# Performance work log

Hardware: AMD Instinct MI355X
Metric: run time of the kernel (lower is better)

## Reference

```python
import jax, jax.numpy as jnp
import numpy as np

U, S, D, ORDER, R, B = 339, 5825, 128, 3, 32, 500000
N = U + S
NNZ = 200000
H = D // 2  # MLP hidden = dimension // 2 = 64
EPS = 1e-5


def _xavier(key, shape):
    lim = (6.0 / (shape[0] + shape[1])) ** 0.5
    return jax.random.uniform(key, shape, minval=-lim, maxval=lim, dtype=jnp.float32)


def setup_inputs() -> dict:
    key = jax.random.key(0)
    ks = jax.random.split(key, 16)
    # --- sparse bipartite adjacency (binary, symmetrized, sym-normalized) ---
    rng = np.random.default_rng(0)
    flat = rng.choice(U * S, size=NNZ, replace=False)
    u = (flat // S).astype(np.int64)
    s = (flat % S).astype(np.int64) + U
    rows = np.concatenate([u, s])
    cols = np.concatenate([s, u])
    deg = np.bincount(rows, minlength=N).astype(np.float32)
    dinv = np.where(deg > 0, deg ** -0.5, 0.0).astype(np.float32)
    vals = dinv[rows] * dinv[cols]
    inp = {
        'uEmbeds': _xavier(ks[0], (U, D)),
        'iEmbeds': _xavier(ks[1], (S, D)),
        'uHyper': _xavier(ks[2], (R, D)),
        'iHyper': _xavier(ks[3], (R, D)),
        'W1': _xavier(ks[4], (2 * D, H)), 'b1': jnp.zeros((H,), jnp.float32),
        'g1': jnp.ones((H,), jnp.float32), 'be1': jnp.zeros((H,), jnp.float32),
        'W2': _xavier(ks[5], (H, H)), 'b2': jnp.zeros((H,), jnp.float32),
        'g2': jnp.ones((H,), jnp.float32), 'be2': jnp.zeros((H,), jnp.float32),
        'W3': _xavier(ks[6], (H, 1)), 'b3': jnp.zeros((1,), jnp.float32),
        'adj_vals': jnp.asarray(vals),
        'adj_rows': jnp.asarray(rows, dtype=jnp.int32),
        'adj_cols': jnp.asarray(cols, dtype=jnp.int32),
        'userIdx': jax.random.randint(ks[7], (B,), 0, U, dtype=jnp.int32),
        'servIdx': jax.random.randint(ks[8], (B,), 0, S, dtype=jnp.int32),
    }
    return inp


def _layernorm(x, g, b):
    mu = jnp.mean(x, axis=-1, keepdims=True)
    var = jnp.var(x, axis=-1, keepdims=True)
    return (x - mu) * jax.lax.rsqrt(var + EPS) * g + b


def reference(uEmbeds, iEmbeds, uHyper, iHyper,
              W1, b1, g1, be1, W2, b2, g2, be2, W3, b3,
              adj_vals, adj_rows, adj_cols, userIdx, servIdx):
    # multi-order GCN propagation via sparse COO spmm
    embeds = jnp.concatenate([uEmbeds, iEmbeds], axis=0)  # [N, D]
    for _ in range(ORDER):
        embeds = jax.ops.segment_sum(adj_vals[:, None] * embeds[adj_cols],
                                     adj_rows, num_segments=N)
    # hypergraph projection (embeds are detached in the original)
    e = jax.lax.stop_gradient(embeds)
    hyperU = e[:U] @ (uHyper.T @ uHyper)   # [U, D]
    hyperI = e[U:] @ (iHyper.T @ iHyper)   # [S, D]
    x = jnp.concatenate([hyperU[userIdx], hyperI[servIdx]], axis=1)  # [B, 2D]
    h = jax.nn.relu(_layernorm(x @ W1 + b1, g1, be1))
    h = jax.nn.relu(_layernorm(h @ W2 + b2, g2, be2))
    return h @ W3 + b3  # [B, 1]
```

## Files before the change

### kernel.cpp

```cpp
#include <hip/hip_runtime.h>
#include <hip/hip_bf16.h>

#define U_CNT 339
#define S_CNT 5825
#define N_CNT 6164
#define D_DIM 128
#define R_DIM 32
#define B_CNT 500000
#define NNZ_U 200000
#define H_DIM 64
#define LN_EPS 1e-5f

#define SPAD 5856
#define UPAD 352
#define KT_S 183
#define KT_U 11
#define NT_S 365
#define NT_U 22
#define U_KCHUNK 23

#define ET_U16 (D_DIM * SPAD)
#define PKS_U16 (KT_U * NT_S * 512)
#define PKU_U16 (KT_S * NT_U * 512)
#define WT_U16  (H_DIM * UPAD)
#define GU_U16  (UPAD * UPAD)
#define V_U16   (KT_U * 8 * 512)

#define PRE_S_UNITS 183
#define PRE_U_UNITS 11
#define PRE_UT_END (PRE_S_UNITS + PRE_U_UNITS)
#define PRE_EDGE_UNITS ((NNZ_U + 255) / 256)
#define PRE_UNITS (PRE_UT_END + PRE_EDGE_UNITS)

#define HV_GU_END 484
#define HV_YT_END 660
#define HV_BLOCKS 669

#define WF_B1   4096
#define WF_G1   4160
#define WF_BE1  4224
#define WF_B2   4288
#define WF_G2   4352
#define WF_BE2  4416
#define WF_W3   4480
#define WF_B3   4544
#define WF_TOT  4545

#define MLP_BLOCKS 1024

typedef __hip_bfloat16 bf16;
typedef __attribute__((ext_vector_type(8))) short sh8;
typedef __attribute__((ext_vector_type(4))) float f4v;

__device__ __forceinline__ float b2f(bf16 x) { return __bfloat162float(x); }
__device__ __forceinline__ unsigned short f2bs(float f) {
    union { bf16 b; unsigned short s; } u;
    u.b = __float2bfloat16(f);
    return u.s;
}
__device__ __forceinline__ float bu2f(unsigned int lo16) {
    return __uint_as_float(lo16 << 16);
}
__device__ __forceinline__ float ldf(const void* p, long i, int isf32) {
    return isf32 ? ((const float*)p)[i] : b2f(((const bf16*)p)[i]);
}
__device__ __forceinline__ int detect_f32(const void* uE) {
    const unsigned short* p = (const unsigned short*)uE;
    int lane = threadIdx.x & 63;
    unsigned short v = p[2 * lane];
    int e = (v >> 7) & 0xFF;
    unsigned long long m = __ballot(e >= 127);
    return (m != 0ull) ? 1 : 0;
}

template<int CTRL>
__device__ __forceinline__ float dpp_add(float x) {
    int t = __builtin_amdgcn_update_dpp(0, __float_as_int(x), CTRL, 0xF, 0xF, false);
    return x + __int_as_float(t);
}
__device__ __forceinline__ float rowsum16(float x) {
    x = dpp_add<0xB1>(x);
    x = dpp_add<0x4E>(x);
    x = dpp_add<0x124>(x);
    x = dpp_add<0x128>(x);
    return x;
}

__global__ void __launch_bounds__(256)
k_pre(const void* __restrict__ iE,
      unsigned short* __restrict__ EtHi, unsigned short* __restrict__ EtLo,
      const int* __restrict__ rows, const int* __restrict__ cols,
      const void* __restrict__ vals,
      unsigned short* __restrict__ PkS, unsigned short* __restrict__ PkU,
      float* __restrict__ uEt,
      const void* __restrict__ uE) {
    __shared__ float ls[32 * 129];
    int tid = threadIdx.x;
    int isf32 = detect_f32(uE);
    int unit = blockIdx.x;
    if (unit < PRE_S_UNITS) {
        int sg0 = unit * 32;
        int nl = tid >> 3, dbase = (tid & 7) * 16;
        int s = sg0 + nl;
        #pragma unroll
        for (int i = 0; i < 16; ++i) {
            int d = dbase + i;
            float v = (s < S_CNT) ? ldf(iE, (long)s * D_DIM + d, isf32) : 0.f;
            ls[nl * 129 + d] = v;
        }
        __syncthreads();
        int nl2 = tid & 31;
        int s2 = sg0 + nl2;
        #pragma unroll
        for (int i = 0; i < 16; ++i) {
            int d = (tid >> 5) * 16 + i;
            float v = ls[nl2 * 129 + d];
            unsigned short hi = f2bs(v);
            unsigned short lo = f2bs(v - bu2f(hi));
            EtHi[(size_t)d * SPAD + s2] = hi;
            EtLo[(size_t)d * SPAD + s2] = lo;
        }
    } else if (unit < PRE_UT_END) {
        int ug0 = (unit - PRE_S_UNITS) * 32;
        int nl = tid >> 3, dbase = (tid & 7) * 16;
        int u = ug0 + nl;
        #pragma unroll
        for (int i = 0; i < 16; ++i) {
            int d = dbase + i;
            float v = (u < U_CNT) ? ldf(uE, (long)u * D_DIM + d, isf32) : 0.f;
            ls[nl * 129 + d] = v;
        }
        __syncthreads();
        int nl2 = tid & 31;
        int u2 = ug0 + nl2;
        #pragma unroll
        for (int i = 0; i < 16; ++i) {
            int d = (tid >> 5) * 16 + i;
            uEt[(size_t)d * UPAD + u2] = (u2 < UPAD) ? ls[nl2 * 129 + d] : 0.f;
        }
    } else {
        int e = (unit - PRE_UT_END) * 256 + tid;
        if (e < NNZ_U) {
            int r = rows[e];
            if (r < U_CNT) {
                int u = r, s = cols[e] - U_CNT;
                unsigned short w = f2bs(ldf(vals, e, isf32));
                int kt = u >> 5, kq = (u >> 3) & 3, j = u & 7;
                int nt = s >> 4, nn = s & 15;
                PkS[((kt * NT_S + nt) * 64 + kq * 16 + nn) * 8 + j] = w;
                int kt2 = s >> 5, kq2 = (s >> 3) & 3, j2 = s & 7;
                int nt2 = u >> 4, nn2 = u & 15;
                PkU[((kt2 * NT_U + nt2) * 64 + kq2 * 16 + nn2) * 8 + j2] = w;
            }
        }
    }
}

__global__ void __launch_bounds__(512)
k_heavy(const unsigned short* __restrict__ EtHi, const unsigned short* __restrict__ EtLo,
        const unsigned short* __restrict__ PkU,
        unsigned short* __restrict__ GuHi, unsigned short* __restrict__ GuLo,
        float* __restrict__ yT,
        const void* __restrict__ uHy, const void* __restrict__ iHy,
        const void* __restrict__ W1, const void* __restrict__ W2,
        const void* __restrict__ b1, const void* __restrict__ g1,
        const void* __restrict__ be1, const void* __restrict__ b2,
        const void* __restrict__ g2, const void* __restrict__ be2,
        const void* __restrict__ W3, const void* __restrict__ b3,
        float* __restrict__ Pc, float* __restrict__ Wf,
        unsigned short* __restrict__ Wb,
        const void* __restrict__ uE) {
    __shared__ __align__(16) float sm[6688];
    int tid = threadIdx.x;
    int bid = blockIdx.x;
    if (bid < HV_YT_END) {
        int wv = tid >> 6, lane = tid & 63;
        int am = lane & 15, aq = lane >> 4;
        const sh8* Bp = (const sh8*)PkU;
        float4* red = (float4*)sm;
        int k0 = wv * U_KCHUNK, k1 = min(KT_S, k0 + U_KCHUNK);
        f4v acc = {0.f, 0.f, 0.f, 0.f};
        int mt, nt;
        if (bid < HV_GU_END) {
            mt = bid / NT_U; nt = bid % NT_U;
            for (int kt = k0; kt < k1; ++kt) {
                sh8 aa = Bp[(kt * NT_U + mt) * 64 + lane];
                sh8 bb = Bp[(kt * NT_U + nt) * 64 + lane];
                acc = __builtin_amdgcn_mfma_f32_16x16x32_bf16(aa, bb, acc, 0, 0, 0);
            }
        } else {
            int tile = bid - HV_GU_END;
            mt = tile / NT_U; nt = tile % NT_U;
            const unsigned short* rH = EtHi + (size_t)(mt * 16 + am) * SPAD;
            const unsigned short* rL = EtLo + (size_t)(mt * 16 + am) * SPAD;
            for (int kt = k0; kt < k1; ++kt) {
                sh8 bb = Bp[(kt * NT_U + nt) * 64 + lane];
                sh8 ah = *(const sh8*)(rH + kt * 32 + aq * 8);
                sh8 al = *(const sh8*)(rL + kt * 32 + aq * 8);
                acc = __builtin_amdgcn_mfma_f32_16x16x32_bf16(ah, bb, acc, 0, 0, 0);
                acc = __builtin_amdgcn_mfma_f32_16x16x32_bf16(al, bb, acc, 0, 0, 0);
            }
        }
        red[wv * 64 + lane] = make_float4(acc[0], acc[1], acc[2], acc[3]);
        __syncthreads();
        if (wv == 0) {
            float4 v = red[lane];
            #pragma unroll
            for (int w2 = 1; w2 < 8; ++w2) {
                float4 p = red[w2 * 64 + lane];
                v.x += p.x; v.y += p.y; v.z += p.z; v.w += p.w;
            }
            float vr[4] = {v.x, v.y, v.z, v.w};
            if (bid < HV_GU_END) {
                #pragma unroll
                for (int reg = 0; reg < 4; ++reg) {
                    size_t idx = (size_t)(mt * 16 + aq * 4 + reg) * UPAD + nt * 16 + am;
                    unsigned short hi = f2bs(vr[reg]);
                    GuHi[idx] = hi;
                    GuLo[idx] = f2bs(vr[reg] - bu2f(hi));
                }
            } else {
                #pragma unroll
                for (int reg = 0; reg < 4; ++reg)
                    yT[(size_t)(mt * 16 + aq * 4 + reg) * UPAD + nt * 16 + am] = vr[reg];
            }
        }
        return;
    }
    int rb = bid - HV_YT_END;
    int isf32 = detect_f32(uE);
    if (rb == 8) {
        for (int i = tid; i < 4096; i += 512) {
            int j = i & 7, lane = (i >> 3) & 63, kh = (i >> 9) & 1, t = i >> 10;
            int k = kh * 32 + ((lane >> 4) & 3) * 8 + j;
            int n = t * 16 + (lane & 15);
            Wb[i] = f2bs(ldf(W2, k * 64 + n, isf32));
        }
        for (int i = tid; i < WF_TOT - 4096; i += 512) {
            int g = 4096 + i;
            float v;
            if      (g < WF_G1)  v = ldf(b1,  g - WF_B1,   isf32);
            else if (g < WF_BE1) v = ldf(g1,  g - WF_G1,   isf32);
            else if (g < WF_B2)  v = ldf(be1, g - WF_BE1,  isf32);
            else if (g < WF_G2)  v = ldf(b2,  g - WF_B2,   isf32);
            else if (g < WF_BE2) v = ldf(g2,  g - WF_G2,   isf32);
            else if (g < WF_W3)  v = ldf(be2, g - WF_BE2,  isf32);
            else if (g < WF_B3)  v = ldf(W3,  g - WF_W3,   isf32);
            else                 v = ldf(b3,  0,           isf32);
            Wf[g] = v;
        }
        return;
    }
    int side = rb >> 2;
    int j0 = (rb & 3) * 16;
    const void* Hy = side ? iHy : uHy;
    long wbase = (long)side * D_DIM * H_DIM;
    float* Hs = sm;
    float* Ws = sm + R_DIM * 129;
    float* Ts = Ws + D_DIM * 16;
    if (isf32) {
        const float* H = (const float*)Hy;
        for (int i = tid; i < R_DIM * D_DIM; i += 512)
            Hs[(i >> 7) * 129 + (i & 127)] = H[i];
        const float* Wp = (const float*)W1 + wbase;
        for (int i = tid; i < D_DIM * 16; i += 512)
            Ws[i] = Wp[(i >> 4) * H_DIM + j0 + (i & 15)];
    } else {
        const unsigned short* H = (const unsigned short*)Hy;
        for (int i = tid; i < R_DIM * D_DIM; i += 512)
            Hs[(i >> 7) * 129 + (i & 127)] = bu2f(H[i]);
        const unsigned short* Wp = (const unsigned short*)W1 + wbase;
        for (int i = tid; i < D_DIM * 16; i += 512)
            Ws[i] = bu2f(Wp[(i >> 4) * H_DIM + j0 + (i & 15)]);
    }
    __syncthreads();
    for (int idx = tid; idx < R_DIM * 16; idx += 512) {
        int a = idx >> 4, j = idx & 15;
        float acc = 0.f;
        #pragma unroll 8
        for (int d = 0; d < D_DIM; ++d)
            acc = fmaf(Hs[a * 129 + d], Ws[d * 16 + j], acc);
        Ts[idx] = acc;
    }
    __syncthreads();
    for (int idx = tid; idx < D_DIM * 16; idx += 512) {
        int d = idx >> 4, j = idx & 15;
        float acc = 0.f;
        #pragma unroll
        for (int a = 0; a < R_DIM; ++a)
            acc = fmaf(Hs[a * 129 + d], Ts[a * 16 + j], acc);
        Pc[side * D_DIM * H_DIM + d * H_DIM + j0 + j] = acc;
    }
}

__global__ void __launch_bounds__(256)
k_midA(const float* __restrict__ yT, const float* __restrict__ uEt,
       const float* __restrict__ Pc,
       unsigned short* __restrict__ VHi, unsigned short* __restrict__ VLo) {
    int bid = blockIdx.x;
    int kt = bid >> 4, jg = bid & 15;
    int tid = threadIdx.x;
    int kl = tid & 31, jl = tid >> 5;
    int k = kt * 32 + kl;
    int j = jg * 8 + jl;
    const float* S = (j < H_DIM) ? yT : uEt;
    const float* P = Pc + ((j < H_DIM) ? (size_t)j
                                       : (size_t)(D_DIM * H_DIM + j - H_DIM));
    float acc = 0.f;
    #pragma unroll 8
    for (int d = 0; d < D_DIM; ++d)
        acc = fmaf(S[(size_t)d * UPAD + k], P[(size_t)d * H_DIM], acc);
    unsigned short hi = f2bs(acc);
    unsigned short lo = f2bs(acc - bu2f(hi));
    int kq = (k >> 3) & 3, jj = k & 7;
    int nt = j >> 4, nn = j & 15;
    size_t idx = ((size_t)(kt * 8 + nt) * 64 + kq * 16 + nn) * 8 + jj;
    VHi[idx] = hi;
    VLo[idx] = lo;
}

__global__ void __launch_bounds__(256)
k_midB(const unsigned short* __restrict__ GuHi, const unsigned short* __restrict__ GuLo,
       const unsigned short* __restrict__ VHi, const unsigned short* __restrict__ VLo,
       const float* __restrict__ Wf, float* __restrict__ A,
       unsigned short* __restrict__ wTH, unsigned short* __restrict__ wTL) {
    int tid = threadIdx.x, wv = tid >> 6, lane = tid & 63;
    int am = lane & 15, aq = lane >> 4;
    int tile = blockIdx.x * 4 + wv;
    int mt = tile >> 3, nt = tile & 7;
    const sh8* BH = (const sh8*)VHi;
    const sh8* BL = (const sh8*)VLo;
    const unsigned short* rH = GuHi + (size_t)(mt * 16 + am) * UPAD;
    const unsigned short* rL = GuLo + (size_t)(mt * 16 + am) * UPAD;
    f4v acc = {0.f, 0.f, 0.f, 0.f};
    #pragma unroll
    for (int kt = 0; kt < KT_U; ++kt) {
        sh8 bh = BH[(kt * 8 + nt) * 64 + lane];
        sh8 bl = BL[(kt * 8 + nt) * 64 + lane];
        sh8 ah = *(const sh8*)(rH + kt * 32 + aq * 8);
        sh8 al = *(const sh8*)(rL + kt * 32 + aq * 8);
        acc = __builtin_amdgcn_mfma_f32_16x16x32_bf16(ah, bh, acc, 0, 0, 0);
        acc = __builtin_amdgcn_mfma_f32_16x16x32_bf16(ah, bl, acc, 0, 0, 0);
        acc = __builtin_amdgcn_mfma_f32_16x16x32_bf16(al, bh, acc, 0, 0, 0);
    }
    if (nt < 4) {
        int j = nt * 16 + am;
        float b1j = Wf[WF_B1 + j];
        #pragma unroll
        for (int reg = 0; reg < 4; ++reg) {
            int r = mt * 16 + aq * 4 + reg;
            if (r < U_CNT) A[(size_t)r * H_DIM + j] = acc[reg] + b1j;
        }
    } else {
        int j = nt * 16 + am - 64;
        int r0 = mt * 16 + aq * 4;
        ushort4 vh, vl;
        unsigned short h;
        h = f2bs(acc[0]); vh.x = h; vl.x = f2bs(acc[0] - bu2f(h));
        h = f2bs(acc[1]); vh.y = h; vl.y = f2bs(acc[1] - bu2f(h));
        h = f2bs(acc[2]); vh.z = h; vl.z = f2bs(acc[2] - bu2f(h));
        h = f2bs(acc[3]); vh.w = h; vl.w = f2bs(acc[3] - bu2f(h));
        *(ushort4*)(wTH + (size_t)j * UPAD + r0) = vh;
        *(ushort4*)(wTL + (size_t)j * UPAD + r0) = vl;
    }
}

__global__ void __launch_bounds__(256)
k_as(const unsigned short* __restrict__ wTH, const unsigned short* __restrict__ wTL,
     const unsigned short* __restrict__ PkS, float* __restrict__ A) {
    __shared__ float ls[16][65];
    int nt = blockIdx.x;
    int tid = threadIdx.x, wv = tid >> 6, lane = tid & 63;
    int am = lane & 15, aq = lane >> 4;
    const sh8* Bp = (const sh8*)PkS;
    const unsigned short* rH = wTH + (size_t)(wv * 16 + am) * UPAD;
    const unsigned short* rL = wTL + (size_t)(wv * 16 + am) * UPAD;
    f4v acc0 = {0.f, 0.f, 0.f, 0.f}, acc1 = acc0;
    #pragma unroll
    for (int kt = 0; kt < KT_U; ++kt) {
        sh8 bb = Bp[(kt * NT_S + nt) * 64 + lane];
        sh8 ah = *(const sh8*)(rH + kt * 32 + aq * 8);
        sh8 al = *(const sh8*)(rL + kt * 32 + aq * 8);
        acc0 = __builtin_amdgcn_mfma_f32_16x16x32_bf16(ah, bb, acc0, 0, 0, 0);
        acc1 = __builtin_amdgcn_mfma_f32_16x16x32_bf16(al, bb, acc1, 0, 0, 0);
    }
    #pragma unroll
    for (int reg = 0; reg < 4; ++reg)
        ls[am][wv * 16 + aq * 4 + reg] = acc0[reg] + acc1[reg];
    __syncthreads();
    int sl = tid >> 4, j0 = (tid & 15) * 4;
    int s = nt * 16 + sl;
    if (s < S_CNT) {
        float4 v = make_float4(ls[sl][j0], ls[sl][j0 + 1], ls[sl][j0 + 2], ls[sl][j0 + 3]);
        *(float4*)(A + (size_t)(U_CNT + s) * H_DIM + j0) = v;
    }
}

__global__ void __launch_bounds__(256)
HyperModel_65755949301857_kernel(
      const float* __restrict__ A, const int* __restrict__ userIdx,
      const int* __restrict__ servIdx, const float* __restrict__ Wf,
      const unsigned short* __restrict__ Wb,
      void* __restrict__ out, const void* __restrict__ uE) {
    int tid = threadIdx.x;
    int wv = tid >> 6, lane = tid & 63;
    int isf32 = detect_f32(uE);
    int m = lane & 15, quad = lane >> 4;

    const sh8* Bp = (const sh8*)Wb;
    sh8 b00 = Bp[0 * 64 + lane], b01 = Bp[1 * 64 + lane];
    sh8 b10 = Bp[2 * 64 + lane], b11 = Bp[3 * 64 + lane];
    sh8 b20 = Bp[4 * 64 + lane], b21 = Bp[5 * 64 + lane];
    sh8 b30 = Bp[6 * 64 + lane], b31 = Bp[7 * 64 + lane];
    float b2c0 = Wf[WF_B2 + m],      b2c1 = Wf[WF_B2 + 16 + m];
    float b2c2 = Wf[WF_B2 + 32 + m], b2c3 = Wf[WF_B2 + 48 + m];
    float g2c0 = Wf[WF_G2 + m],      g2c1 = Wf[WF_G2 + 16 + m];
    float g2c2 = Wf[WF_G2 + 32 + m], g2c3 = Wf[WF_G2 + 48 + m];
    float e2c0 = Wf[WF_BE2 + m],      e2c1 = Wf[WF_BE2 + 16 + m];
    float e2c2 = Wf[WF_BE2 + 32 + m], e2c3 = Wf[WF_BE2 + 48 + m];
    float w3c0 = Wf[WF_W3 + m],      w3c1 = Wf[WF_W3 + 16 + m];
    float w3c2 = Wf[WF_W3 + 32 + m], w3c3 = Wf[WF_W3 + 48 + m];
    float b3v = Wf[WF_B3];
    const float* G1l = Wf + WF_G1 + quad * 8;
    const float* BE1l = Wf + WF_BE1 + quad * 8;

    const long TILES = B_CNT / 16;
    const long stride = (long)gridDim.x * 4;
    long tile = (long)blockIdx.x * 4 + wv;
    if (tile >= TILES) return;

    int r0 = (int)(tile * 16 + m);
    const float4* Au = (const float4*)(A + (long)userIdx[r0] * 64);
    const float4* As = (const float4*)(A + (long)(servIdx[r0] + U_CNT) * 64);
    float4 bu0 = Au[quad * 2], bu1 = Au[quad * 2 + 1], bu2 = Au[8 + quad * 2], bu3 = Au[9 + quad * 2];
    float4 bs0 = As[quad * 2], bs1 = As[quad * 2 + 1], bs2 = As[8 + quad * 2], bs3 = As[9 + quad * 2];
    long tn = tile + stride;
    int uin = 0, sin = 0;
    if (tn < TILES) {
        int rn = (int)(tn * 16 + m);
        uin = userIdx[rn];
        sin = servIdx[rn] + U_CNT;
    }

    while (true) {
        float zl[8], zh[8];
        zl[0] = bu0.x + bs0.x; zl[1] = bu0.y + bs0.y; zl[2] = bu0.z + bs0.z; zl[3] = bu0.w + bs0.w;
        zl[4] = bu1.x + bs1.x; zl[5] = bu1.y + bs1.y; zl[6] = bu1.z + bs1.z; zl[7] = bu1.w + bs1.w;
        zh[0] = bu2.x + bs2.x; zh[1] = bu2.y + bs2.y; zh[2] = bu2.z + bs2.z; zh[3] = bu2.w + bs2.w;
        zh[4] = bu3.x + bs3.x; zh[5] = bu3.y + bs3.y; zh[6] = bu3.z + bs3.z; zh[7] = bu3.w + bs3.w;

        long tcur = tile;
        bool have_next = (tn < TILES);
        if (have_next) {
            const float4* Au2 = (const float4*)(A + (long)uin * 64);
            const float4* As2 = (const float4*)(A + (long)sin * 64);
            bu0 = Au2[quad * 2]; bu1 = Au2[quad * 2 + 1]; bu2 = Au2[8 + quad * 2]; bu3 = Au2[9 + quad * 2];
            bs0 = As2[quad * 2]; bs1 = As2[quad * 2 + 1]; bs2 = As2[8 + quad * 2]; bs3 = As2[9 + quad * 2];
            long tnn = tn + stride;
            if (tnn < TILES) {
                int rnn = (int)(tnn * 16 + m);
                uin = userIdx[rnn];
                sin = servIdx[rnn] + U_CNT;
            }
            tile = tn;
            tn = tnn;
        }

        float s = 0.f, q = 0.f;
        #pragma unroll
        for (int j = 0; j < 8; ++j) {
            s += zl[j] + zh[j];
            q = fmaf(zl[j], zl[j], q);
            q = fmaf(zh[j], zh[j], q);
        }
        s += __shfl_xor(s, 16, 64); s += __shfl_xor(s, 32, 64);
        q += __shfl_xor(q, 16, 64); q += __shfl_xor(q, 32, 64);
        float mu = s * (1.f / 64.f);
        float rs = rsqrtf(q * (1.f / 64.f) - mu * mu + LN_EPS);
        float nm = -mu * rs;

        sh8 a0, a1;
        #pragma unroll
        for (int j = 0; j < 8; ++j) {
            float h0 = fmaxf(fmaf(fmaf(zl[j], rs, nm), G1l[j],      BE1l[j]),      0.f);
            float h1 = fmaxf(fmaf(fmaf(zh[j], rs, nm), G1l[32 + j], BE1l[32 + j]), 0.f);
            a0[j] = (short)f2bs(h0);
            a1[j] = (short)f2bs(h1);
        }

        f4v acc0 = {0.f, 0.f, 0.f, 0.f}, acc1 = acc0, acc2 = acc0, acc3 = acc0;
        acc0 = __builtin_amdgcn_mfma_f32_16x16x32_bf16(a0, b00, acc0, 0, 0, 0);
        acc0 = __builtin_amdgcn_mfma_f32_16x16x32_bf16(a1, b01, acc0, 0, 0, 0);
        acc1 = __builtin_amdgcn_mfma_f32_16x16x32_bf16(a0, b10, acc1, 0, 0, 0);
        acc1 = __builtin_amdgcn_mfma_f32_16x16x32_bf16(a1, b11, acc1, 0, 0, 0);
        acc2 = __builtin_amdgcn_mfma_f32_16x16x32_bf16(a0, b20, acc2, 0, 0, 0);
        acc2 = __builtin_amdgcn_mfma_f32_16x16x32_bf16(a1, b21, acc2, 0, 0, 0);
        acc3 = __builtin_amdgcn_mfma_f32_16x16x32_bf16(a0, b30, acc3, 0, 0, 0);
        acc3 = __builtin_amdgcn_mfma_f32_16x16x32_bf16(a1, b31, acc3, 0, 0, 0);

        float y0[4], y1[4], y2[4], y3[4];
        float srow[4], qrow[4];
        #pragma unroll
        for (int reg = 0; reg < 4; ++reg) {
            y0[reg] = acc0[reg] + b2c0;
            y1[reg] = acc1[reg] + b2c1;
            y2[reg] = acc2[reg] + b2c2;
            y3[reg] = acc3[reg] + b2c3;
            srow[reg] = (y0[reg] + y1[reg]) + (y2[reg] + y3[reg]);
            float qa = y0[reg] * y0[reg];
            qa = fmaf(y1[reg], y1[reg], qa);
            qa = fmaf(y2[reg], y2[reg], qa);
            qa = fmaf(y3[reg], y3[reg], qa);
            qrow[reg] = qa;
        }
        #pragma unroll
        for (int reg = 0; reg < 4; ++reg) {
            srow[reg] = rowsum16(srow[reg]);
            qrow[reg] = rowsum16(qrow[reg]);
        }
        float o[4];
        #pragma unroll
        for (int reg = 0; reg < 4; ++reg) {
            float mu2 = srow[reg] * (1.f / 64.f);
            float rs2 = rsqrtf(qrow[reg] * (1.f / 64.f) - mu2 * mu2 + LN_EPS);
            float nm2 = -mu2 * rs2;
            float t0 = fmaxf(fmaf(fmaf(y0[reg], rs2, nm2), g2c0, e2c0), 0.f);
            float t1 = fmaxf(fmaf(fmaf(y1[reg], rs2, nm2), g2c1, e2c1), 0.f);
            float t2 = fmaxf(fmaf(fmaf(y2[reg], rs2, nm2), g2c2, e2c2), 0.f);
            float t3 = fmaxf(fmaf(fmaf(y3[reg], rs2, nm2), g2c3, e2c3), 0.f);
            o[reg] = fmaf(t0, w3c0, fmaf(t1, w3c1, fmaf(t2, w3c2, t3 * w3c3)));
        }
        #pragma unroll
        for (int reg = 0; reg < 4; ++reg) o[reg] = rowsum16(o[reg]);
        if (m == 0) {
            long rb = tcur * 16 + quad * 4;
            if (isf32) {
                float4 v = make_float4(o[0] + b3v, o[1] + b3v, o[2] + b3v, o[3] + b3v);
                *(float4*)((float*)out + rb) = v;
            } else {
                ushort4 v;
                v.x = f2bs(o[0] + b3v);
                v.y = f2bs(o[1] + b3v);
                v.z = f2bs(o[2] + b3v);
                v.w = f2bs(o[3] + b3v);
                *(ushort4*)((bf16*)out + rb) = v;
            }
        }
        if (!have_next) break;
    }
}

extern "C" __attribute__((visibility("default")))
void kernel_launch(void* const* d_in, const int* in_sizes, int n_in,
                   void* d_out, int out_size, void* d_ws, size_t ws_size,
                   hipStream_t stream) {
    const void* uE   = d_in[0];
    const void* iE   = d_in[1];
    const void* uHy  = d_in[2];
    const void* iHy  = d_in[3];
    const void* W1   = d_in[4];
    const void* b1   = d_in[5];
    const void* g1   = d_in[6];
    const void* be1  = d_in[7];
    const void* W2   = d_in[8];
    const void* b2   = d_in[9];
    const void* g2   = d_in[10];
    const void* be2  = d_in[11];
    const void* W3   = d_in[12];
    const void* b3   = d_in[13];
    const void* adj_vals = d_in[14];
    const int*  adj_rows = (const int*)d_in[15];
    const int*  adj_cols = (const int*)d_in[16];
    const int*  userIdx  = (const int*)d_in[17];
    const int*  servIdx  = (const int*)d_in[18];

    char* w = (char*)d_ws;
    size_t off = 0;
    auto alloc = [&](size_t bytes) -> char* {
        char* p = w + off;
        off += (bytes + 255) & ~(size_t)255;
        return p;
    };
    unsigned short* EtHi = (unsigned short*)alloc((size_t)ET_U16 * 2);
    unsigned short* EtLo = (unsigned short*)alloc((size_t)ET_U16 * 2);
    unsigned short* GuHi = (unsigned short*)alloc((size_t)GU_U16 * 2);
    unsigned short* GuLo = (unsigned short*)alloc((size_t)GU_U16 * 2);
    unsigned short* VHi  = (unsigned short*)alloc((size_t)V_U16 * 2);
    unsigned short* VLo  = (unsigned short*)alloc((size_t)V_U16 * 2);
    unsigned short* wTH  = (unsigned short*)alloc((size_t)WT_U16 * 2);
    unsigned short* wTL  = (unsigned short*)alloc((size_t)WT_U16 * 2);
    float* yT   = (float*)alloc((size_t)D_DIM * UPAD * 4);
    float* uEt  = (float*)alloc((size_t)D_DIM * UPAD * 4);
    float* Pc   = (float*)alloc((size_t)2 * D_DIM * H_DIM * 4);
    float* A    = (float*)alloc((size_t)N_CNT * H_DIM * 4);
    float* Wf   = (float*)alloc((size_t)WF_TOT * 4);
    unsigned short* Wb = (unsigned short*)alloc((size_t)4096 * 2);
    unsigned short* PkS = (unsigned short*)alloc((size_t)PKS_U16 * 2);
    unsigned short* PkU = (unsigned short*)alloc((size_t)PKU_U16 * 2);
    size_t zspan = (size_t)((char*)(PkU + PKU_U16) - (char*)PkS);

    hipMemsetAsync(PkS, 0, zspan, stream);
    k_pre<<<PRE_UNITS, 256, 0, stream>>>(iE, EtHi, EtLo, adj_rows, adj_cols,
                                         adj_vals, PkS, PkU, uEt, uE);
    k_heavy<<<HV_BLOCKS, 512, 0, stream>>>(EtHi, EtLo, PkU, GuHi, GuLo, yT,
                                           uHy, iHy, W1, W2, b1, g1, be1,
                                           b2, g2, be2, W3, b3,
                                           Pc, Wf, Wb, uE);
    k_midA<<<176, 256, 0, stream>>>(yT, uEt, Pc, VHi, VLo);
    k_midB<<<44, 256, 0, stream>>>(GuHi, GuLo, VHi, VLo, Wf, A, wTH, wTL);
    k_as<<<NT_S, 256, 0, stream>>>(wTH, wTL, PkS, A);
    HyperModel_65755949301857_kernel<<<MLP_BLOCKS, 256, 0, stream>>>(
        A, userIdx, servIdx, Wf, Wb, d_out, uE);
}
```

Baseline: 181.2 us.

## Exploit Gu symmetry, move weight prep to k_pre, pair tiles in k_as

The user Gram matrix tiles are now computed only for the lower triangle (253 instead of 484 blocks), and each result is mirror-written to the transposed position. The hyper-projection and MLP weight packing blocks move from k_heavy into k_pre, where they run alongside the edge scatter. k_as now processes two column tiles per block so the A fragments are shared, and the MLP grid grows to 1280 blocks. The triangle index decode with sqrt and the strided transpose stores add a little overhead, and the final k_as block has only one tile.

```diff
diff --git a/kernel.cpp b/kernel.cpp
--- a/kernel.cpp
+++ b/kernel.cpp
@@ -30,11 +30,12 @@
 #define PRE_U_UNITS 11
 #define PRE_UT_END (PRE_S_UNITS + PRE_U_UNITS)
 #define PRE_EDGE_UNITS ((NNZ_U + 255) / 256)
-#define PRE_UNITS (PRE_UT_END + PRE_EDGE_UNITS)
-
-#define HV_GU_END 484
-#define HV_YT_END 660
-#define HV_BLOCKS 669
+#define PRE_EDGE_END (PRE_UT_END + PRE_EDGE_UNITS)
+#define PRE_UNITS (PRE_EDGE_END + 9)
+
+#define HV_GU_END 253
+#define HV_YT_END 429
+#define HV_BLOCKS 429
 
 #define WF_B1   4096
 #define WF_G1   4160
@@ -46,7 +47,7 @@
 #define WF_B3   4544
 #define WF_TOT  4545
 
-#define MLP_BLOCKS 1024
+#define MLP_BLOCKS 1280
 
 typedef __hip_bfloat16 bf16;
 typedef __attribute__((ext_vector_type(8))) short sh8;
@@ -93,12 +94,21 @@
       const void* __restrict__ vals,
       unsigned short* __restrict__ PkS, unsigned short* __restrict__ PkU,
       float* __restrict__ uEt,
+      const void* __restrict__ uHy, const void* __restrict__ iHy,
+      const void* __restrict__ W1, const void* __restrict__ W2,
+      const void* __restrict__ b1, const void* __restrict__ g1,
+      const void* __restrict__ be1, const void* __restrict__ b2,
+      const void* __restrict__ g2, const void* __restrict__ be2,
+      const void* __restrict__ W3, const void* __restrict__ b3,
+      float* __restrict__ Pc, float* __restrict__ Wf,
+      unsigned short* __restrict__ Wb,
       const void* __restrict__ uE) {
-    __shared__ float ls[32 * 129];
+    __shared__ __align__(16) float sm[6688];
     int tid = threadIdx.x;
     int isf32 = detect_f32(uE);
     int unit = blockIdx.x;
     if (unit < PRE_S_UNITS) {
+        float* ls = sm;
         int sg0 = unit * 32;
         int nl = tid >> 3, dbase = (tid & 7) * 16;
         int s = sg0 + nl;
@@ -121,6 +131,7 @@
             EtLo[(size_t)d * SPAD + s2] = lo;
         }
     } else if (unit < PRE_UT_END) {
+        float* ls = sm;
         int ug0 = (unit - PRE_S_UNITS) * 32;
         int nl = tid >> 3, dbase = (tid & 7) * 16;
         int u = ug0 + nl;
@@ -136,9 +147,9 @@
         #pragma unroll
         for (int i = 0; i < 16; ++i) {
             int d = (tid >> 5) * 16 + i;
-            uEt[(size_t)d * UPAD + u2] = (u2 < UPAD) ? ls[nl2 * 129 + d] : 0.f;
-        }
-    } else {
+            uEt[(size_t)d * UPAD + u2] = ls[nl2 * 129 + d];
+        }
+    } else if (unit < PRE_EDGE_END) {
         int e = (unit - PRE_UT_END) * 256 + tid;
         if (e < NNZ_U) {
             int r = rows[e];
@@ -153,6 +164,70 @@
                 PkU[((kt2 * NT_U + nt2) * 64 + kq2 * 16 + nn2) * 8 + j2] = w;
             }
         }
+    } else {
+        int rb = unit - PRE_EDGE_END;
+        if (rb == 8) {
+            for (int i = tid; i < 4096; i += 256) {
+                int j = i & 7, lane = (i >> 3) & 63, kh = (i >> 9) & 1, t = i >> 10;
+                int k = kh * 32 + ((lane >> 4) & 3) * 8 + j;
+                int n = t * 16 + (lane & 15);
+                Wb[i] = f2bs(ldf(W2, k * 64 + n, isf32));
+            }
+            for (int i = tid; i < WF_TOT - 4096; i += 256) {
+                int g = 4096 + i;
+                float v;
+                if      (g < WF_G1)  v = ldf(b1,  g - WF_B1,   isf32);
+                else if (g < WF_BE1) v = ldf(g1,  g - WF_G1,   isf32);
+                else if (g < WF_B2)  v = ldf(be1, g - WF_BE1,  isf32);
+                else if (g < WF_G2)  v = ldf(b2,  g - WF_B2,   isf32);
+                else if (g < WF_BE2) v = ldf(g2,  g - WF_G2,   isf32);
+                else if (g < WF_W3)  v = ldf(be2, g - WF_BE2,  isf32);
+                else if (g < WF_B3)  v = ldf(W3,  g - WF_W3,   isf32);
+                else                 v = ldf(b3,  0,           isf32);
+                Wf[g] = v;
+            }
+            return;
+        }
+        int side = rb >> 2;
+        int j0 = (rb & 3) * 16;
+        const void* Hy = side ? iHy : uHy;
+        long wbase = (long)side * D_DIM * H_DIM;
+        float* Hs = sm;
+        float* Ws = sm + R_DIM * 129;
+        float* Ts = Ws + D_DIM * 16;
+        if (isf32) {
+            const float* H = (const float*)Hy;
+            for (int i = tid; i < R_DIM * D_DIM; i += 256)
+                Hs[(i >> 7) * 129 + (i & 127)] = H[i];
+            const float* Wp = (const float*)W1 + wbase;
+            for (int i = tid; i < D_DIM * 16; i += 256)
+                Ws[i] = Wp[(i >> 4) * H_DIM + j0 + (i & 15)];
+        } else {
+            const unsigned short* H = (const unsigned short*)Hy;
+            for (int i = tid; i < R_DIM * D_DIM; i += 256)
+                Hs[(i >> 7) * 129 + (i & 127)] = bu2f(H[i]);
+            const unsigned short* Wp = (const unsigned short*)W1 + wbase;
+            for (int i = tid; i < D_DIM * 16; i += 256)
+                Ws[i] = bu2f(Wp[(i >> 4) * H_DIM + j0 + (i & 15)]);
+        }
+        __syncthreads();
+        for (int idx = tid; idx < R_DIM * 16; idx += 256) {
+            int a = idx >> 4, j = idx & 15;
+            float acc = 0.f;
+            #pragma unroll 8
+            for (int d = 0; d < D_DIM; ++d)
+                acc = fmaf(Hs[a * 129 + d], Ws[d * 16 + j], acc);
+            Ts[idx] = acc;
+        }
+        __syncthreads();
+        for (int idx = tid; idx < D_DIM * 16; idx += 256) {
+            int d = idx >> 4, j = idx & 15;
+            float acc = 0.f;
+            #pragma unroll
+            for (int a = 0; a < R_DIM; ++a)
+                acc = fmaf(Hs[a * 129 + d], Ts[a * 16 + j], acc);
+            Pc[side * D_DIM * H_DIM + d * H_DIM + j0 + j] = acc;
+        }
     }
 }
 
@@ -160,136 +235,74 @@
 k_heavy(const unsigned short* __restrict__ EtHi, const unsigned short* __restrict__ EtLo,
         const unsigned short* __restrict__ PkU,
         unsigned short* __restrict__ GuHi, unsigned short* __restrict__ GuLo,
-        float* __restrict__ yT,
-        const void* __restrict__ uHy, const void* __restrict__ iHy,
-        const void* __restrict__ W1, const void* __restrict__ W2,
-        const void* __restrict__ b1, const void* __restrict__ g1,
-        const void* __restrict__ be1, const void* __restrict__ b2,
-        const void* __restrict__ g2, const void* __restrict__ be2,
-        const void* __restrict__ W3, const void* __restrict__ b3,
-        float* __restrict__ Pc, float* __restrict__ Wf,
-        unsigned short* __restrict__ Wb,
-        const void* __restrict__ uE) {
-    __shared__ __align__(16) float sm[6688];
+        float* __restrict__ yT) {
+    __shared__ __align__(16) float4 red[512];
     int tid = threadIdx.x;
     int bid = blockIdx.x;
-    if (bid < HV_YT_END) {
-        int wv = tid >> 6, lane = tid & 63;
-        int am = lane & 15, aq = lane >> 4;
-        const sh8* Bp = (const sh8*)PkU;
-        float4* red = (float4*)sm;
-        int k0 = wv * U_KCHUNK, k1 = min(KT_S, k0 + U_KCHUNK);
-        f4v acc = {0.f, 0.f, 0.f, 0.f};
-        int mt, nt;
+    int wv = tid >> 6, lane = tid & 63;
+    int am = lane & 15, aq = lane >> 4;
+    const sh8* Bp = (const sh8*)PkU;
+    int k0 = wv * U_KCHUNK, k1 = min(KT_S, k0 + U_KCHUNK);
+    f4v acc = {0.f, 0.f, 0.f, 0.f};
+    int mt, nt;
+    if (bid < HV_GU_END) {
+        mt = (int)((sqrtf(8.f * (float)bid + 1.f) - 1.f) * 0.5f);
+        while ((mt + 1) * (mt + 2) / 2 <= bid) ++mt;
+        while (mt * (mt + 1) / 2 > bid) --mt;
+        nt = bid - mt * (mt + 1) / 2;
+        for (int kt = k0; kt < k1; ++kt) {
+            sh8 aa = Bp[(kt * NT_U + mt) * 64 + lane];
+            sh8 bb = Bp[(kt * NT_U + nt) * 64 + lane];
+            acc = __builtin_amdgcn_mfma_f32_16x16x32_bf16(aa, bb, acc, 0, 0, 0);
+        }
+    } else {
+        int tile = bid - HV_GU_END;
+        mt = tile / NT_U; nt = tile % NT_U;
+        const unsigned short* rH = EtHi + (size_t)(mt * 16 + am) * SPAD;
+        const unsigned short* rL = EtLo + (size_t)(mt * 16 + am) * SPAD;
+        for (int kt = k0; kt < k1; ++kt) {
+            sh8 bb = Bp[(kt * NT_U + nt) * 64 + lane];
+            sh8 ah = *(const sh8*)(rH + kt * 32 + aq * 8);
+            sh8 al = *(const sh8*)(rL + kt * 32 + aq * 8);
+            acc = __builtin_amdgcn_mfma_f32_16x16x32_bf16(ah, bb, acc, 0, 0, 0);
+            acc = __builtin_amdgcn_mfma_f32_16x16x32_bf16(al, bb, acc, 0, 0, 0);
+        }
+    }
+    red[wv * 64 + lane] = make_float4(acc[0], acc[1], acc[2], acc[3]);
+    __syncthreads();
+    if (wv == 0) {
+        float4 v = red[lane];
+        #pragma unroll
+        for (int w2 = 1; w2 < 8; ++w2) {
+            float4 p = red[w2 * 64 + lane];
+            v.x += p.x; v.y += p.y; v.z += p.z; v.w += p.w;
+        }
+        float vr[4] = {v.x, v.y, v.z, v.w};
         if (bid < HV_GU_END) {
-            mt = bid / NT_U; nt = bid % NT_U;
-            for (int kt = k0; kt < k1; ++kt) {
-                sh8 aa = Bp[(kt * NT_U + mt) * 64 + lane];
-                sh8 bb = Bp[(kt * NT_U + nt) * 64 + lane];
-                acc = __builtin_amdgcn_mfma_f32_16x16x32_bf16(aa, bb, acc, 0, 0, 0);
+            ushort4 mh, ml;
+            unsigned short h;
+            h = f2bs(vr[0]); mh.x = h; ml.x = f2bs(vr[0] - bu2f(h));
+            h = f2bs(vr[1]); mh.y = h; ml.y = f2bs(vr[1] - bu2f(h));
+            h = f2bs(vr[2]); mh.z = h; ml.z = f2bs(vr[2] - bu2f(h));
+            h = f2bs(vr[3]); mh.w = h; ml.w = f2bs(vr[3] - bu2f(h));
+            unsigned short hv[4] = {mh.x, mh.y, mh.z, mh.w};
+            unsigned short lv[4] = {ml.x, ml.y, ml.z, ml.w};
+            #pragma unroll
+            for (int reg = 0; reg < 4; ++reg) {
+                size_t idx = (size_t)(mt * 16 + aq * 4 + reg) * UPAD + nt * 16 + am;
+                GuHi[idx] = hv[reg];
+                GuLo[idx] = lv[reg];
+            }
+            if (mt != nt) {
+                size_t mi = (size_t)(nt * 16 + am) * UPAD + mt * 16 + aq * 4;
+                *(ushort4*)(GuHi + mi) = mh;
+                *(ushort4*)(GuLo + mi) = ml;
             }
         } else {
-            int tile = bid - HV_GU_END;
-            mt = tile / NT_U; nt = tile % NT_U;
-            const unsigned short* rH = EtHi + (size_t)(mt * 16 + am) * SPAD;
-            const unsigned short* rL = EtLo + (size_t)(mt * 16 + am) * SPAD;
-            for (int kt = k0; kt < k1; ++kt) {
-                sh8 bb = Bp[(kt * NT_U + nt) * 64 + lane];
-                sh8 ah = *(const sh8*)(rH + kt * 32 + aq * 8);
-                sh8 al = *(const sh8*)(rL + kt * 32 + aq * 8);
-                acc = __builtin_amdgcn_mfma_f32_16x16x32_bf16(ah, bb, acc, 0, 0, 0);
-                acc = __builtin_amdgcn_mfma_f32_16x16x32_bf16(al, bb, acc, 0, 0, 0);
-            }
-        }
-        red[wv * 64 + lane] = make_float4(acc[0], acc[1], acc[2], acc[3]);
-        __syncthreads();
-        if (wv == 0) {
-            float4 v = red[lane];
             #pragma unroll
-            for (int w2 = 1; w2 < 8; ++w2) {
-                float4 p = red[w2 * 64 + lane];
-                v.x += p.x; v.y += p.y; v.z += p.z; v.w += p.w;
-            }
-            float vr[4] = {v.x, v.y, v.z, v.w};
-            if (bid < HV_GU_END) {
-                #pragma unroll
-                for (int reg = 0; reg < 4; ++reg) {
-                    size_t idx = (size_t)(mt * 16 + aq * 4 + reg) * UPAD + nt * 16 + am;
-                    unsigned short hi = f2bs(vr[reg]);
-                    GuHi[idx] = hi;
-                    GuLo[idx] = f2bs(vr[reg] - bu2f(hi));
-                }
-            } else {
-                #pragma unroll
-                for (int reg = 0; reg < 4; ++reg)
-                    yT[(size_t)(mt * 16 + aq * 4 + reg) * UPAD + nt * 16 + am] = vr[reg];
-            }
-        }
-        return;
-    }
-    int rb = bid - HV_YT_END;
-    int isf32 = detect_f32(uE);
-    if (rb == 8) {
-        for (int i = tid; i < 4096; i += 512) {
-            int j = i & 7, lane = (i >> 3) & 63, kh = (i >> 9) & 1, t = i >> 10;
-            int k = kh * 32 + ((lane >> 4) & 3) * 8 + j;
-            int n = t * 16 + (lane & 15);
-            Wb[i] = f2bs(ldf(W2, k * 64 + n, isf32));
-        }
-        for (int i = tid; i < WF_TOT - 4096; i += 512) {
-            int g = 4096 + i;
-            float v;
-            if      (g < WF_G1)  v = ldf(b1,  g - WF_B1,   isf32);
-            else if (g < WF_BE1) v = ldf(g1,  g - WF_G1,   isf32);
-            else if (g < WF_B2)  v = ldf(be1, g - WF_BE1,  isf32);
-            else if (g < WF_G2)  v = ldf(b2,  g - WF_B2,   isf32);
-            else if (g < WF_BE2) v = ldf(g2,  g - WF_G2,   isf32);
-            else if (g < WF_W3)  v = ldf(be2, g - WF_BE2,  isf32);
-            else if (g < WF_B3)  v = ldf(W3,  g - WF_W3,   isf32);
-            else                 v = ldf(b3,  0,           isf32);
-            Wf[g] = v;
-        }
-        return;
-    }
-    int side = rb >> 2;
-    int j0 = (rb & 3) * 16;
-    const void* Hy = side ? iHy : uHy;
-    long wbase = (long)side * D_DIM * H_DIM;
-    float* Hs = sm;
-    float* Ws = sm + R_DIM * 129;
-    float* Ts = Ws + D_DIM * 16;
-    if (isf32) {
-        const float* H = (const float*)Hy;
-        for (int i = tid; i < R_DIM * D_DIM; i += 512)
-            Hs[(i >> 7) * 129 + (i & 127)] = H[i];
-        const float* Wp = (const float*)W1 + wbase;
-        for (int i = tid; i < D_DIM * 16; i += 512)
-            Ws[i] = Wp[(i >> 4) * H_DIM + j0 + (i & 15)];
-    } else {
-        const unsigned short* H = (const unsigned short*)Hy;
-        for (int i = tid; i < R_DIM * D_DIM; i += 512)
-            Hs[(i >> 7) * 129 + (i & 127)] = bu2f(H[i]);
-        const unsigned short* Wp = (const unsigned short*)W1 + wbase;
-        for (int i = tid; i < D_DIM * 16; i += 512)
-            Ws[i] = bu2f(Wp[(i >> 4) * H_DIM + j0 + (i & 15)]);
-    }
-    __syncthreads();
-    for (int idx = tid; idx < R_DIM * 16; idx += 512) {
-        int a = idx >> 4, j = idx & 15;
-        float acc = 0.f;
-        #pragma unroll 8
-        for (int d = 0; d < D_DIM; ++d)
-            acc = fmaf(Hs[a * 129 + d], Ws[d * 16 + j], acc);
-        Ts[idx] = acc;
-    }
-    __syncthreads();
-    for (int idx = tid; idx < D_DIM * 16; idx += 512) {
-        int d = idx >> 4, j = idx & 15;
-        float acc = 0.f;
-        #pragma unroll
-        for (int a = 0; a < R_DIM; ++a)
-            acc = fmaf(Hs[a * 129 + d], Ts[a * 16 + j], acc);
-        Pc[side * D_DIM * H_DIM + d * H_DIM + j0 + j] = acc;
+            for (int reg = 0; reg < 4; ++reg)
+                yT[(size_t)(mt * 16 + aq * 4 + reg) * UPAD + nt * 16 + am] = vr[reg];
+        }
     }
 }
 
@@ -368,31 +381,43 @@
 __global__ void __launch_bounds__(256)
 k_as(const unsigned short* __restrict__ wTH, const unsigned short* __restrict__ wTL,
      const unsigned short* __restrict__ PkS, float* __restrict__ A) {
-    __shared__ float ls[16][65];
-    int nt = blockIdx.x;
+    __shared__ float ls[2][16][65];
+    int nt0 = blockIdx.x * 2;
+    int has2 = (nt0 + 1 < NT_S);
     int tid = threadIdx.x, wv = tid >> 6, lane = tid & 63;
     int am = lane & 15, aq = lane >> 4;
     const sh8* Bp = (const sh8*)PkS;
     const unsigned short* rH = wTH + (size_t)(wv * 16 + am) * UPAD;
     const unsigned short* rL = wTL + (size_t)(wv * 16 + am) * UPAD;
-    f4v acc0 = {0.f, 0.f, 0.f, 0.f}, acc1 = acc0;
+    f4v a0h = {0.f, 0.f, 0.f, 0.f}, a0l = a0h, a1h = a0h, a1l = a0h;
     #pragma unroll
     for (int kt = 0; kt < KT_U; ++kt) {
-        sh8 bb = Bp[(kt * NT_S + nt) * 64 + lane];
         sh8 ah = *(const sh8*)(rH + kt * 32 + aq * 8);
         sh8 al = *(const sh8*)(rL + kt * 32 + aq * 8);
-        acc0 = __builtin_amdgcn_mfma_f32_16x16x32_bf16(ah, bb, acc0, 0, 0, 0);
-        acc1 = __builtin_amdgcn_mfma_f32_16x16x32_bf16(al, bb, acc1, 0, 0, 0);
+        sh8 bb0 = Bp[(kt * NT_S + nt0) * 64 + lane];
+        a0h = __builtin_amdgcn_mfma_f32_16x16x32_bf16(ah, bb0, a0h, 0, 0, 0);
+        a0l = __builtin_amdgcn_mfma_f32_16x16x32_bf16(al, bb0, a0l, 0, 0, 0);
+        if (has2) {
+            sh8 bb1 = Bp[(kt * NT_S + nt0 + 1) * 64 + lane];
+            a1h = __builtin_amdgcn_mfma_f32_16x16x32_bf16(ah, bb1, a1h, 0, 0, 0);
+            a1l = __builtin_amdgcn_mfma_f32_16x16x32_bf16(al, bb1, a1l, 0, 0, 0);
+        }
     }
     #pragma unroll
-    for (int reg = 0; reg < 4; ++reg)
-        ls[am][wv * 16 + aq * 4 + reg] = acc0[reg] + acc1[reg];
+    for (int reg = 0; reg < 4; ++reg) {
+        ls[0][am][wv * 16 + aq * 4 + reg] = a0h[reg] + a0l[reg];
+        ls[1][am][wv * 16 + aq * 4 + reg] = a1h[reg] + a1l[reg];
+    }
     __syncthreads();
     int sl = tid >> 4, j0 = (tid & 15) * 4;
-    int s = nt * 16 + sl;
-    if (s < S_CNT) {
-        float4 v = make_float4(ls[sl][j0], ls[sl][j0 + 1], ls[sl][j0 + 2], ls[sl][j0 + 3]);
-        *(float4*)(A + (size_t)(U_CNT + s) * H_DIM + j0) = v;
+    #pragma unroll
+    for (int g = 0; g < 2; ++g) {
+        int s = (nt0 + g) * 16 + sl;
+        if ((g == 0 || has2) && s < S_CNT) {
+            float4 v = make_float4(ls[g][sl][j0], ls[g][sl][j0 + 1],
+                                   ls[g][sl][j0 + 2], ls[g][sl][j0 + 3]);
+            *(float4*)(A + (size_t)(U_CNT + s) * H_DIM + j0) = v;
+        }
     }
 }
 
@@ -601,14 +626,13 @@
 
     hipMemsetAsync(PkS, 0, zspan, stream);
     k_pre<<<PRE_UNITS, 256, 0, stream>>>(iE, EtHi, EtLo, adj_rows, adj_cols,
-                                         adj_vals, PkS, PkU, uEt, uE);
-    k_heavy<<<HV_BLOCKS, 512, 0, stream>>>(EtHi, EtLo, PkU, GuHi, GuLo, yT,
-                                           uHy, iHy, W1, W2, b1, g1, be1,
-                                           b2, g2, be2, W3, b3,
-                                           Pc, Wf, Wb, uE);
+                                         adj_vals, PkS, PkU, uEt,
+                                         uHy, iHy, W1, W2, b1, g1, be1,
+                                         b2, g2, be2, W3, b3, Pc, Wf, Wb, uE);
+    k_heavy<<<HV_BLOCKS, 512, 0, stream>>>(EtHi, EtLo, PkU, GuHi, GuLo, yT);
     k_midA<<<176, 256, 0, stream>>>(yT, uEt, Pc, VHi, VLo);
     k_midB<<<44, 256, 0, stream>>>(GuHi, GuLo, VHi, VLo, Wf, A, wTH, wTL);
-    k_as<<<NT_S, 256, 0, stream>>>(wTH, wTL, PkS, A);
+    k_as<<<183, 256, 0, stream>>>(wTH, wTL, PkS, A);
     HyperModel_65755949301857_kernel<<<MLP_BLOCKS, 256, 0, stream>>>(
         A, userIdx, servIdx, Wf, Wb, d_out, uE);
 }
```

Result: slower. 187.2 us (+3.3%).
